# Kernel optimization log

Hardware: AMD Instinct MI355X
Metric: run time of the kernel (lower is better)

Reference implementation:

```python
import jax, jax.numpy as jnp
import numpy as np

B, S, D, H = 16, 4096, 1024, 1024
VOCAB = 512
EMB_DIM = 3


def setup_inputs() -> dict:
    key = jax.random.key(0)
    ks = jax.random.split(key, 12)
    sd = 1.0 / np.sqrt(D)
    sh = 1.0 / np.sqrt(H)
    return {
        "hs": jax.random.normal(ks[0], (B, S, D), dtype=jnp.float32),
        "ht_k": jax.random.normal(ks[1], (B, D), dtype=jnp.float32),
        "hm_k": jax.random.normal(ks[2], (B, H), dtype=jnp.float32),
        "Ws_w": jax.random.uniform(ks[3], (H, D), jnp.float32, -sd, sd),
        "Ws_b": jax.random.uniform(ks[4], (H,), jnp.float32, -sd, sd),
        "Wt_w": jax.random.uniform(ks[5], (H, D), jnp.float32, -sd, sd),
        "Wt_b": jax.random.uniform(ks[6], (H,), jnp.float32, -sd, sd),
        "Wr_w": jax.random.uniform(ks[7], (H, H), jnp.float32, -sh, sh),
        "Wr_b": jax.random.uniform(ks[8], (H,), jnp.float32, -sh, sh),
        "We_w": jax.random.uniform(ks[9], (H,), jnp.float32, -sh, sh),
        "We_b": jax.random.uniform(ks[10], (1,), jnp.float32, -sh, sh),
        "emb_table": jax.random.normal(ks[11], (VOCAB * VOCAB, EMB_DIM), dtype=jnp.float32),
        "entity_lambda": jnp.array([0.3, 0.5, 0.2], dtype=jnp.float32),
        "hs_i": jax.random.randint(jax.random.fold_in(key, 100), (B, S), 0, VOCAB),
        "ht_k_i": jax.random.randint(jax.random.fold_in(key, 101), (B,), 0, VOCAB),
    }


def reference(hs, ht_k, hm_k, Ws_w, Ws_b, Wt_w, Wt_b, Wr_w, Wr_b, We_w, We_b,
              emb_table, entity_lambda, hs_i, ht_k_i):
    # Projections
    W_hs = jnp.einsum('bsd,hd->bsh', hs, Ws_w) + Ws_b          # [B,S,H]
    W_ht = (ht_k @ Wt_w.T + Wt_b)[:, None, :]                   # [B,1,H]
    W_hm = (hm_k @ Wr_w.T + Wr_b)[:, None, :]                   # [B,1,H]
    # Additive attention score
    W_sum = jnp.tanh(W_hs + W_ht + W_hm) @ We_w + We_b[0]       # [B,S]
    # Relative-position bias: gather then contract with lambda
    rel_pos = hs_i * VOCAB + ht_k_i[:, None]                    # [B,S]
    rel_value = emb_table[rel_pos] @ entity_lambda              # [B,S]
    W_sum = W_sum + rel_value
    # Softmax over sequence, weighted sum of projected source states
    W_softmax = jax.nn.softmax(W_sum, axis=1)                   # [B,S]
    alpha = jnp.einsum('bs,bsh->bh', W_softmax, W_hs)           # [B,H]
    return alpha
```

## Files before the change

kernel.cpp:

```cpp
#include <hip/hip_runtime.h>
#include <hip/hip_bf16.h>
#include <cstdint>
#include <cstddef>

typedef __attribute__((ext_vector_type(4))) float f32x4;
typedef __attribute__((ext_vector_type(8))) short short8;

#define S_LEN 4096
#define D_DIM 1024
#define H_DIM 1024
#define B_SZ  16
#define M_TOT (B_SZ * S_LEN)
#define NT 32

__device__ __forceinline__ unsigned short f2bf(float f) {
  unsigned int u = __float_as_uint(f);
  u += 0x7fffu + ((u >> 16) & 1u);
  return (unsigned short)(u >> 16);
}

__device__ __forceinline__ void gload_lds16(void* lds, const void* g) {
  __builtin_amdgcn_global_load_lds(
      (const __attribute__((address_space(1))) unsigned int*)g,
      (__attribute__((address_space(3))) unsigned int*)lds, 16, 0, 0);
}

__device__ __forceinline__ float tanh_fast(float x) {
  return 1.0f - 2.0f / (1.0f + __expf(2.0f * x));
}

#define WAITV(N) asm volatile("s_waitcnt vmcnt(" #N ")" ::: "memory")
#define BAR() __builtin_amdgcn_s_barrier()

__global__ void cvt_hs_kernel(const float* __restrict__ w,
                              unsigned short* __restrict__ o) {
  size_t i = ((size_t)blockIdx.x * 256 + threadIdx.x) * 8;
  float4 v0 = *(const float4*)(w + i);
  float4 v1 = *(const float4*)(w + i + 4);
  union { unsigned short us[8]; short8 v; } pk;
  pk.us[0] = f2bf(v0.x); pk.us[1] = f2bf(v0.y);
  pk.us[2] = f2bf(v0.z); pk.us[3] = f2bf(v0.w);
  pk.us[4] = f2bf(v1.x); pk.us[5] = f2bf(v1.y);
  pk.us[6] = f2bf(v1.z); pk.us[7] = f2bf(v1.w);
  *(short8*)(o + i) = pk.v;
}

__global__ void cvt_w_kernel(const float* __restrict__ w,
                             unsigned short* __restrict__ o) {
  int i = (blockIdx.x * 256 + threadIdx.x) * 8;
  float4 v0 = *(const float4*)(w + i);
  float4 v1 = *(const float4*)(w + i + 4);
  union { unsigned short us[8]; short8 v; } pk;
  pk.us[0] = f2bf(v0.x); pk.us[1] = f2bf(v0.y);
  pk.us[2] = f2bf(v0.z); pk.us[3] = f2bf(v0.w);
  pk.us[4] = f2bf(v1.x); pk.us[5] = f2bf(v1.y);
  pk.us[6] = f2bf(v1.z); pk.us[7] = f2bf(v1.w);
  *(short8*)(o + i) = pk.v;
}

__global__ void prep_c_kernel(const float* __restrict__ ht,
                              const float* __restrict__ hm,
                              const float* __restrict__ Wt_w,
                              const float* __restrict__ Wt_b,
                              const float* __restrict__ Wr_w,
                              const float* __restrict__ Wr_b,
                              float* __restrict__ cvec) {
  int gw = blockIdx.x * 4 + (threadIdx.x >> 6);
  int lane = threadIdx.x & 63;
  int b = gw >> 10;
  int h = gw & 1023;
  const float* a1 = ht + b * D_DIM;
  const float* w1 = Wt_w + (size_t)h * D_DIM;
  const float* a2 = hm + b * H_DIM;
  const float* w2 = Wr_w + (size_t)h * H_DIM;
  float acc = 0.f;
#pragma unroll
  for (int i = 0; i < 4; ++i) {
    int d = lane * 4 + i * 256;
    float4 x1 = *(const float4*)(a1 + d);
    float4 y1 = *(const float4*)(w1 + d);
    float4 x2 = *(const float4*)(a2 + d);
    float4 y2 = *(const float4*)(w2 + d);
    acc += x1.x * y1.x + x1.y * y1.y + x1.z * y1.z + x1.w * y1.w;
    acc += x2.x * y2.x + x2.y * y2.y + x2.z * y2.z + x2.w * y2.w;
  }
#pragma unroll
  for (int off = 32; off >= 1; off >>= 1) acc += __shfl_xor(acc, off);
  if (lane == 0) cvec[b * H_DIM + h] = acc + Wt_b[h] + Wr_b[h];
}

__device__ __forceinline__ void issue_tile(int kt, int tid,
                                           unsigned short* lA,
                                           unsigned short* lB,
                                           const unsigned short* pA0,
                                           const unsigned short* pA1,
                                           const unsigned short* pB0,
                                           const unsigned short* pB1) {
  const int bq = (kt & 3) * 8192;
  const int ko = kt * 32;
  gload_lds16(&lA[bq + tid * 8], pA0 + ko);
  gload_lds16(&lA[bq + 4096 + tid * 8], pA1 + ko);
  gload_lds16(&lB[bq + tid * 8], pB0 + ko);
  gload_lds16(&lB[bq + 4096 + tid * 8], pB1 + ko);
}

__device__ __forceinline__ void read_frags(const unsigned short* bufA,
                                           const unsigned short* bufB,
                                           int aoff0, int boff0,
                                           short8 (&fa)[8], short8 (&fb)[4]) {
#pragma unroll
  for (int ni = 0; ni < 4; ++ni)
    fb[ni] = *(const short8*)(bufB + boff0 + ni * 512);
#pragma unroll
  for (int mi = 0; mi < 8; ++mi)
    fa[mi] = *(const short8*)(bufA + aoff0 + mi * 512);
}

__device__ __forceinline__ void mfma32(const short8 (&fa)[8],
                                       const short8 (&fb)[4],
                                       f32x4 (&acc)[8][4]) {
  __builtin_amdgcn_s_setprio(1);
#pragma unroll
  for (int mi = 0; mi < 8; ++mi)
#pragma unroll
    for (int ni = 0; ni < 4; ++ni)
      acc[mi][ni] = __builtin_amdgcn_mfma_f32_16x16x32_bf16(
          fa[mi], fb[ni], acc[mi][ni], 0, 0, 0);
  __builtin_amdgcn_s_setprio(0);
}

__global__ __launch_bounds__(512, 2) void score_gemm2_kernel(
    const unsigned short* __restrict__ hsb,
    const unsigned short* __restrict__ Wsb,
    const float* __restrict__ cvec,
    const float* __restrict__ We_w,
    float* __restrict__ score_part) {
  extern __shared__ unsigned short dynls[];
  unsigned short* lA = dynls;
  unsigned short* lB = dynls + 32768;
  __shared__ float scorebuf[4][256];

  const int tid = threadIdx.x;
  const int lane = tid & 63;
  const int wave = tid >> 6;
  const int wm = wave >> 2;
  const int wn = wave & 3;
  const int l15 = lane & 15;
  const int lg = lane >> 4;

  int d = blockIdx.x;
  int tileid = (d & 7) * 128 + (d >> 3);
  const int mtile = tileid >> 2;
  const int nc = tileid & 3;
  const int m0 = mtile * 256;
  const int n0 = nc * 256;
  const int b = m0 >> 12;

  const int r0 = tid >> 2;
  const int r1 = 128 + r0;
  const int sp = tid & 3;
  const int c0 = (sp ^ ((r0 >> 1) & 3)) * 8;
  const int c1 = (sp ^ ((r1 >> 1) & 3)) * 8;
  const unsigned short* pA0 = hsb + (size_t)(m0 + r0) * D_DIM + c0;
  const unsigned short* pA1 = hsb + (size_t)(m0 + r1) * D_DIM + c1;
  const unsigned short* pB0 = Wsb + (size_t)(n0 + r0) * D_DIM + c0;
  const unsigned short* pB1 = Wsb + (size_t)(n0 + r1) * D_DIM + c1;

  const int arow0 = wm * 128 + l15;
  const int aoff0 = arow0 * 32 + (lg ^ ((arow0 >> 1) & 3)) * 8;
  const int brow0 = wn * 64 + l15;
  const int boff0 = brow0 * 32 + (lg ^ ((brow0 >> 1) & 3)) * 8;

  f32x4 acc[8][4];
#pragma unroll
  for (int i = 0; i < 8; ++i)
#pragma unroll
    for (int j = 0; j < 4; ++j) acc[i][j] = (f32x4){0.f, 0.f, 0.f, 0.f};

  short8 fa0[8], fb0[4], fa1[8], fb1[4];

  issue_tile(0, tid, lA, lB, pA0, pA1, pB0, pB1);
  issue_tile(1, tid, lA, lB, pA0, pA1, pB0, pB1);
  issue_tile(2, tid, lA, lB, pA0, pA1, pB0, pB1);
  WAITV(4);
  BAR();
  read_frags(lA, lB, aoff0, boff0, fa0, fb0);

  for (int kt = 0; kt < NT - 4; kt += 2) {
    issue_tile(kt + 3, tid, lA, lB, pA0, pA1, pB0, pB1);
    {
      int bq = ((kt + 1) & 3) * 8192;
      read_frags(lA + bq, lB + bq, aoff0, boff0, fa1, fb1);
    }
    mfma32(fa0, fb0, acc);
    WAITV(4);
    BAR();
    issue_tile(kt + 4, tid, lA, lB, pA0, pA1, pB0, pB1);
    {
      int bq = ((kt + 2) & 3) * 8192;
      read_frags(lA + bq, lB + bq, aoff0, boff0, fa0, fb0);
    }
    mfma32(fa1, fb1, acc);
    WAITV(4);
    BAR();
  }
  issue_tile(NT - 1, tid, lA, lB, pA0, pA1, pB0, pB1);
  {
    int bq = ((NT - 3) & 3) * 8192;
    read_frags(lA + bq, lB + bq, aoff0, boff0, fa1, fb1);
  }
  mfma32(fa0, fb0, acc);
  WAITV(4);
  BAR();
  {
    int bq = ((NT - 2) & 3) * 8192;
    read_frags(lA + bq, lB + bq, aoff0, boff0, fa0, fb0);
  }
  mfma32(fa1, fb1, acc);
  WAITV(0);
  BAR();
  {
    int bq = ((NT - 1) & 3) * 8192;
    read_frags(lA + bq, lB + bq, aoff0, boff0, fa1, fb1);
  }
  mfma32(fa0, fb0, acc);
  mfma32(fa1, fb1, acc);

  float chv[4], whv[4];
#pragma unroll
  for (int ni = 0; ni < 4; ++ni) {
    int h = n0 + wn * 64 + ni * 16 + l15;
    chv[ni] = cvec[b * H_DIM + h];
    whv[ni] = We_w[h];
  }
#pragma unroll
  for (int mi = 0; mi < 8; ++mi)
#pragma unroll
    for (int r = 0; r < 4; ++r) {
      float s = 0.f;
#pragma unroll
      for (int ni = 0; ni < 4; ++ni)
        s += tanh_fast(acc[mi][ni][r] + chv[ni]) * whv[ni];
      s += __shfl_xor(s, 1);
      s += __shfl_xor(s, 2);
      s += __shfl_xor(s, 4);
      s += __shfl_xor(s, 8);
      if (l15 == 0) scorebuf[wn][wm * 128 + mi * 16 + lg * 4 + r] = s;
    }
  __syncthreads();
  if (tid < 256) {
    float s = scorebuf[0][tid] + scorebuf[1][tid] + scorebuf[2][tid] +
              scorebuf[3][tid];
    score_part[(size_t)nc * M_TOT + m0 + tid] = s;
  }
}

__global__ __launch_bounds__(256) void score_gemm_fp32_kernel(
    const float* __restrict__ hs,
    const unsigned short* __restrict__ Wsb,
    const float* __restrict__ cvec,
    const float* __restrict__ We_w,
    float* __restrict__ score_part) {
  __shared__ __align__(16) unsigned short lA[128 * 64];
  __shared__ __align__(16) unsigned short lB[128 * 64];
  __shared__ float scorebuf[2][128];

  const int tid = threadIdx.x;
  const int lane = tid & 63;
  const int wave = tid >> 6;
  const int wr = wave >> 1;
  const int wc = wave & 1;
  const int mtile = blockIdx.x;
  const int gy = blockIdx.y;
  const int m0 = mtile * 128;
  const int b = mtile >> 5;
  const int l15 = lane & 15;
  const int lg = lane >> 4;

  float rowsum[4][4];
#pragma unroll
  for (int i = 0; i < 4; ++i)
#pragma unroll
    for (int j = 0; j < 4; ++j) rowsum[i][j] = 0.f;

  for (int ncq = gy * 4; ncq < gy * 4 + 4; ++ncq) {
    const int n0 = ncq * 128;
    f32x4 acc[4][4];
#pragma unroll
    for (int i = 0; i < 4; ++i)
#pragma unroll
      for (int j = 0; j < 4; ++j) acc[i][j] = (f32x4){0.f, 0.f, 0.f, 0.f};

    for (int k0 = 0; k0 < D_DIM; k0 += 64) {
#pragma unroll
      for (int r = 0; r < 4; ++r) {
        int s = tid + r * 256;
        int row = s >> 3, sl = s & 7;
        int src = sl ^ (row & 7);
        gload_lds16(&lB[s * 8], Wsb + (size_t)(n0 + row) * D_DIM + k0 + src * 8);
      }
      float4 a0[4], a1[4];
#pragma unroll
      for (int r = 0; r < 4; ++r) {
        int s = tid + r * 256;
        int row = s >> 3, sl = s & 7;
        int src = sl ^ (row & 7);
        const float* ga = hs + (size_t)(m0 + row) * D_DIM + k0 + src * 8;
        a0[r] = *(const float4*)ga;
        a1[r] = *(const float4*)(ga + 4);
      }
#pragma unroll
      for (int r = 0; r < 4; ++r) {
        int s = tid + r * 256;
        union { unsigned short us[8]; short8 v; } pk;
        pk.us[0] = f2bf(a0[r].x); pk.us[1] = f2bf(a0[r].y);
        pk.us[2] = f2bf(a0[r].z); pk.us[3] = f2bf(a0[r].w);
        pk.us[4] = f2bf(a1[r].x); pk.us[5] = f2bf(a1[r].y);
        pk.us[6] = f2bf(a1[r].z); pk.us[7] = f2bf(a1[r].w);
        *(short8*)(&lA[s * 8]) = pk.v;
      }
      __syncthreads();
#pragma unroll
      for (int kf = 0; kf < 2; ++kf) {
        short8 af[4], bfr[4];
        int cgrp = kf * 4 + lg;
#pragma unroll
        for (int mi = 0; mi < 4; ++mi) {
          int row = wr * 64 + mi * 16 + l15;
          af[mi] = *(const short8*)&lA[row * 64 + (cgrp ^ (row & 7)) * 8];
        }
#pragma unroll
        for (int ni = 0; ni < 4; ++ni) {
          int row = wc * 64 + ni * 16 + l15;
          bfr[ni] = *(const short8*)&lB[row * 64 + (cgrp ^ (row & 7)) * 8];
        }
#pragma unroll
        for (int mi = 0; mi < 4; ++mi)
#pragma unroll
          for (int ni = 0; ni < 4; ++ni)
            acc[mi][ni] = __builtin_amdgcn_mfma_f32_16x16x32_bf16(
                af[mi], bfr[ni], acc[mi][ni], 0, 0, 0);
      }
      __syncthreads();
    }
#pragma unroll
    for (int ni = 0; ni < 4; ++ni) {
      int h = n0 + wc * 64 + ni * 16 + l15;
      float ch = cvec[b * H_DIM + h];
      float wh = We_w[h];
#pragma unroll
      for (int mi = 0; mi < 4; ++mi)
#pragma unroll
        for (int r2 = 0; r2 < 4; ++r2)
          rowsum[mi][r2] += tanh_fast(acc[mi][ni][r2] + ch) * wh;
    }
  }
#pragma unroll
  for (int mi = 0; mi < 4; ++mi)
#pragma unroll
    for (int r2 = 0; r2 < 4; ++r2) {
      float v = rowsum[mi][r2];
      v += __shfl_xor(v, 1);
      v += __shfl_xor(v, 2);
      v += __shfl_xor(v, 4);
      v += __shfl_xor(v, 8);
      rowsum[mi][r2] = v;
    }
  if (l15 == 0) {
#pragma unroll
    for (int mi = 0; mi < 4; ++mi)
#pragma unroll
      for (int r2 = 0; r2 < 4; ++r2)
        scorebuf[wc][wr * 64 + mi * 16 + lg * 4 + r2] = rowsum[mi][r2];
  }
  __syncthreads();
  if (tid < 128) {
    score_part[(size_t)gy * M_TOT + m0 + tid] =
        scorebuf[0][tid] + scorebuf[1][tid];
  }
}

__global__ void softmax_kernel(const float* __restrict__ part,
                               const int* __restrict__ hs_i,
                               const int* __restrict__ ht_i,
                               const float* __restrict__ emb,
                               const float* __restrict__ lam,
                               float* __restrict__ wout, int nparts) {
  int b = blockIdx.x;
  int tid = threadIdx.x;
  float lam0 = lam[0], lam1 = lam[1], lam2 = lam[2];
  int tk = ht_i[b];
  float xs[16];
  float mx = -1e30f;
#pragma unroll
  for (int i = 0; i < 16; ++i) {
    int s = tid + i * 256;
    size_t m = (size_t)b * S_LEN + s;
    float x = 0.f;
    for (int g = 0; g < nparts; ++g) x += part[(size_t)g * M_TOT + m];
    int idx = hs_i[m] * 512 + tk;
    const float* e = emb + (size_t)idx * 3;
    x += e[0] * lam0 + e[1] * lam1 + e[2] * lam2;
    xs[i] = x;
    mx = fmaxf(mx, x);
  }
  __shared__ float redm[4];
  __shared__ float reds[4];
#pragma unroll
  for (int off = 32; off >= 1; off >>= 1) mx = fmaxf(mx, __shfl_xor(mx, off));
  if ((tid & 63) == 0) redm[tid >> 6] = mx;
  __syncthreads();
  mx = fmaxf(fmaxf(redm[0], redm[1]), fmaxf(redm[2], redm[3]));
  float sum = 0.f;
#pragma unroll
  for (int i = 0; i < 16; ++i) {
    xs[i] = __expf(xs[i] - mx);
    sum += xs[i];
  }
#pragma unroll
  for (int off = 32; off >= 1; off >>= 1) sum += __shfl_xor(sum, off);
  if ((tid & 63) == 0) reds[tid >> 6] = sum;
  __syncthreads();
  sum = reds[0] + reds[1] + reds[2] + reds[3];
  float inv = 1.0f / sum;
#pragma unroll
  for (int i = 0; i < 16; ++i)
    wout[(size_t)b * S_LEN + tid + i * 256] = xs[i] * inv;
}

__global__ void wsum_bf16_kernel(const unsigned short* __restrict__ hsb,
                                 const float* __restrict__ w,
                                 float* __restrict__ u) {
  int bx = blockIdx.x;
  int b = bx >> 5;
  int sc = bx & 31;
  int tid = threadIdx.x;
  int dcol = tid * 4;
  int s0 = sc * 128;
  const unsigned short* base = hsb + ((size_t)b * S_LEN + s0) * D_DIM + dcol;
  const float* wrow = w + (size_t)b * S_LEN + s0;
  float4 acc = {0.f, 0.f, 0.f, 0.f};
#pragma unroll 4
  for (int i = 0; i < 128; ++i) {
    float ww = wrow[i];
    ushort2 v01 = *(const ushort2*)(base + (size_t)i * D_DIM);
    ushort2 v23 = *(const ushort2*)(base + (size_t)i * D_DIM + 2);
    acc.x += ww * __uint_as_float((unsigned int)v01.x << 16);
    acc.y += ww * __uint_as_float((unsigned int)v01.y << 16);
    acc.z += ww * __uint_as_float((unsigned int)v23.x << 16);
    acc.w += ww * __uint_as_float((unsigned int)v23.y << 16);
  }
  atomicAdd(&u[b * D_DIM + dcol + 0], acc.x);
  atomicAdd(&u[b * D_DIM + dcol + 1], acc.y);
  atomicAdd(&u[b * D_DIM + dcol + 2], acc.z);
  atomicAdd(&u[b * D_DIM + dcol + 3], acc.w);
}

__global__ void wsum_kernel(const float* __restrict__ hs,
                            const float* __restrict__ w,
                            float* __restrict__ u) {
  int bx = blockIdx.x;
  int b = bx >> 5;
  int sc = bx & 31;
  int tid = threadIdx.x;
  int dcol = tid * 4;
  int s0 = sc * 128;
  const float* base = hs + ((size_t)b * S_LEN + s0) * D_DIM + dcol;
  const float* wrow = w + (size_t)b * S_LEN + s0;
  float4 acc = {0.f, 0.f, 0.f, 0.f};
#pragma unroll 4
  for (int i = 0; i < 128; ++i) {
    float ww = wrow[i];
    float4 v = *(const float4*)(base + (size_t)i * D_DIM);
    acc.x += ww * v.x;
    acc.y += ww * v.y;
    acc.z += ww * v.z;
    acc.w += ww * v.w;
  }
  atomicAdd(&u[b * D_DIM + dcol + 0], acc.x);
  atomicAdd(&u[b * D_DIM + dcol + 1], acc.y);
  atomicAdd(&u[b * D_DIM + dcol + 2], acc.z);
  atomicAdd(&u[b * D_DIM + dcol + 3], acc.w);
}

__global__ void alpha_kernel(const float* __restrict__ u,
                             const float* __restrict__ Ws_w,
                             const float* __restrict__ Ws_b,
                             float* __restrict__ out) {
  int gw = blockIdx.x * 4 + (threadIdx.x >> 6);
  int lane = threadIdx.x & 63;
  int b = gw >> 10;
  int h = gw & 1023;
  const float* ur = u + b * D_DIM;
  const float* wrow = Ws_w + (size_t)h * D_DIM;
  float acc = 0.f;
#pragma unroll
  for (int i = 0; i < 4; ++i) {
    int dcol = lane * 4 + i * 256;
    float4 x = *(const float4*)(ur + dcol);
    float4 y = *(const float4*)(wrow + dcol);
    acc += x.x * y.x + x.y * y.y + x.z * y.z + x.w * y.w;
  }
#pragma unroll
  for (int off = 32; off >= 1; off >>= 1) acc += __shfl_xor(acc, off);
  if (lane == 0) out[b * H_DIM + h] = acc + Ws_b[h];
}

extern "C" void kernel_launch(void* const* d_in, const int* in_sizes, int n_in,
                              void* d_out, int out_size, void* d_ws,
                              size_t ws_size, hipStream_t stream) {
  const float* hs = (const float*)d_in[0];
  const float* ht_k = (const float*)d_in[1];
  const float* hm_k = (const float*)d_in[2];
  const float* Ws_w = (const float*)d_in[3];
  const float* Ws_b = (const float*)d_in[4];
  const float* Wt_w = (const float*)d_in[5];
  const float* Wt_b = (const float*)d_in[6];
  const float* Wr_w = (const float*)d_in[7];
  const float* Wr_b = (const float*)d_in[8];
  const float* We_w = (const float*)d_in[9];
  const float* emb = (const float*)d_in[11];
  const float* lam = (const float*)d_in[12];
  const int* hs_i = (const int*)d_in[13];
  const int* ht_i = (const int*)d_in[14];
  float* out = (float*)d_out;

  const size_t HSB = (size_t)M_TOT * D_DIM * 2;
  const size_t FAST_NEEDED = HSB + 2097152 + 1048576 + 262144 + 65536 + 65536;

  char* ws = (char*)d_ws;
  if (ws_size >= FAST_NEEDED) {
    unsigned short* hsb = (unsigned short*)ws;
    unsigned short* Wsb = (unsigned short*)(ws + HSB);
    float* part = (float*)(ws + HSB + 2097152);
    float* wgt = (float*)(ws + HSB + 2097152 + 1048576);
    float* u = (float*)(ws + HSB + 2097152 + 1048576 + 262144);
    float* cvec = (float*)(ws + HSB + 2097152 + 1048576 + 262144 + 65536);

    hipFuncSetAttribute((const void*)score_gemm2_kernel,
                        hipFuncAttributeMaxDynamicSharedMemorySize, 131072);

    cvt_hs_kernel<<<32768, 256, 0, stream>>>(hs, hsb);
    cvt_w_kernel<<<512, 256, 0, stream>>>(Ws_w, Wsb);
    prep_c_kernel<<<4096, 256, 0, stream>>>(ht_k, hm_k, Wt_w, Wt_b, Wr_w,
                                            Wr_b, cvec);
    score_gemm2_kernel<<<1024, 512, 131072, stream>>>(hsb, Wsb, cvec, We_w,
                                                      part);
    softmax_kernel<<<16, 256, 0, stream>>>(part, hs_i, ht_i, emb, lam, wgt, 4);
    hipMemsetAsync(u, 0, B_SZ * D_DIM * sizeof(float), stream);
    wsum_bf16_kernel<<<512, 256, 0, stream>>>(hsb, wgt, u);
    alpha_kernel<<<4096, 256, 0, stream>>>(u, Ws_w, Ws_b, out);
    return;
  }

  unsigned short* Wsb = (unsigned short*)(ws);
  float* cvec = (float*)(ws + 2097152);
  float* part = (float*)(ws + 2097152 + 65536);
  float* wgt = (float*)(ws + 2097152 + 65536 + 524288);
  float* u = (float*)(ws + 2097152 + 65536 + 524288 + 262144);

  cvt_w_kernel<<<512, 256, 0, stream>>>(Ws_w, Wsb);
  prep_c_kernel<<<4096, 256, 0, stream>>>(ht_k, hm_k, Wt_w, Wt_b, Wr_w, Wr_b,
                                          cvec);
  dim3 g2(512, 2);
  score_gemm_fp32_kernel<<<g2, 256, 0, stream>>>(hs, Wsb, cvec, We_w, part);
  softmax_kernel<<<16, 256, 0, stream>>>(part, hs_i, ht_i, emb, lam, wgt, 2);
  hipMemsetAsync(u, 0, B_SZ * D_DIM * sizeof(float), stream);
  wsum_kernel<<<512, 256, 0, stream>>>(hs, wgt, u);
  alpha_kernel<<<4096, 256, 0, stream>>>(u, Ws_w, Ws_b, out);
}
```

Before: 299.3 us.

## Restructure score GEMM main loop to double-buffered K=64 stages with interleaved loads

Replaces the 4-deep ring of K=32 tiles with a 2-buffer scheme of K=64 stages (16 iterations), using a new XOR swizzle over 8 column chunks. Each stage is split into four quarter-steps, each issuing a slice of the next stage's global-to-LDS loads, reading fragments, waiting on lgkmcnt and running 16 MFMAs. The goal is to spread load issue evenly across the compute and cut register pressure from double fragment sets. In exchange it adds many more barriers per stage and a full vmcnt(0) drain at the end of each stage, which shortens the prefetch distance.

```diff
diff --git a/kernel.cpp b/kernel.cpp
--- a/kernel.cpp
+++ b/kernel.cpp
@@ -11,7 +11,6 @@
 #define H_DIM 1024
 #define B_SZ  16
 #define M_TOT (B_SZ * S_LEN)
-#define NT 32
 
 __device__ __forceinline__ unsigned short f2bf(float f) {
   unsigned int u = __float_as_uint(f);
@@ -29,8 +28,12 @@
   return 1.0f - 2.0f / (1.0f + __expf(2.0f * x));
 }
 
-#define WAITV(N) asm volatile("s_waitcnt vmcnt(" #N ")" ::: "memory")
 #define BAR() __builtin_amdgcn_s_barrier()
+#define LGKM0()                                            \
+  do {                                                     \
+    asm volatile("s_waitcnt lgkmcnt(0)" ::: "memory");     \
+    __builtin_amdgcn_sched_barrier(0);                     \
+  } while (0)
 
 __global__ void cvt_hs_kernel(const float* __restrict__ w,
                               unsigned short* __restrict__ o) {
@@ -89,47 +92,44 @@
   if (lane == 0) cvec[b * H_DIM + h] = acc + Wt_b[h] + Wr_b[h];
 }
 
-__device__ __forceinline__ void issue_tile(int kt, int tid,
-                                           unsigned short* lA,
-                                           unsigned short* lB,
-                                           const unsigned short* pA0,
-                                           const unsigned short* pA1,
-                                           const unsigned short* pB0,
-                                           const unsigned short* pB1) {
-  const int bq = (kt & 3) * 8192;
-  const int ko = kt * 32;
-  gload_lds16(&lA[bq + tid * 8], pA0 + ko);
-  gload_lds16(&lA[bq + 4096 + tid * 8], pA1 + ko);
-  gload_lds16(&lB[bq + tid * 8], pB0 + ko);
-  gload_lds16(&lB[bq + 4096 + tid * 8], pB1 + ko);
-}
-
-__device__ __forceinline__ void read_frags(const unsigned short* bufA,
-                                           const unsigned short* bufB,
-                                           int aoff0, int boff0,
-                                           short8 (&fa)[8], short8 (&fb)[4]) {
-#pragma unroll
-  for (int ni = 0; ni < 4; ++ni)
-    fb[ni] = *(const short8*)(bufB + boff0 + ni * 512);
-#pragma unroll
-  for (int mi = 0; mi < 8; ++mi)
-    fa[mi] = *(const short8*)(bufA + aoff0 + mi * 512);
-}
-
-__device__ __forceinline__ void mfma32(const short8 (&fa)[8],
-                                       const short8 (&fb)[4],
-                                       f32x4 (&acc)[8][4]) {
-  __builtin_amdgcn_s_setprio(1);
-#pragma unroll
-  for (int mi = 0; mi < 8; ++mi)
-#pragma unroll
-    for (int ni = 0; ni < 4; ++ni)
-      acc[mi][ni] = __builtin_amdgcn_mfma_f32_16x16x32_bf16(
-          fa[mi], fb[ni], acc[mi][ni], 0, 0, 0);
-  __builtin_amdgcn_s_setprio(0);
-}
-
-__global__ __launch_bounds__(512, 2) void score_gemm2_kernel(
+#define STG_A(nb, h, ss)                                                  \
+  do {                                                                    \
+    gload_lds16(lA + (nb)*16384 + (h)*8192 + dst0,                        \
+                gA + (h)*131072 + (ss)*64);                               \
+    gload_lds16(lA + (nb)*16384 + (h)*8192 + dst1,                        \
+                gA + (h)*131072 + 65536 + (ss)*64);                       \
+  } while (0)
+#define STG_B(nb, h, ss)                                                  \
+  do {                                                                    \
+    gload_lds16(lB + (nb)*16384 + (h)*8192 + dst0,                        \
+                gB + (h)*131072 + (ss)*64);                               \
+    gload_lds16(lB + (nb)*16384 + (h)*8192 + dst1,                        \
+                gB + (h)*131072 + 65536 + (ss)*64);                       \
+  } while (0)
+
+#define RDA_LO(OFF)                                                       \
+  { _Pragma("unroll") for (int mi = 0; mi < 4; ++mi)                      \
+      fa[mi] = *(const short8*)(bA + (OFF) + mi * 1024); }
+#define RDA_HI(OFF)                                                       \
+  { _Pragma("unroll") for (int mi = 0; mi < 4; ++mi)                      \
+      fa[mi] = *(const short8*)(bA + (OFF) + 4096 + mi * 1024); }
+#define RDB(FB, OFF)                                                      \
+  { _Pragma("unroll") for (int ni = 0; ni < 4; ++ni)                      \
+      FB[ni] = *(const short8*)(bB + (OFF) + ni * 1024); }
+
+#define MM16(MIB, FB)                                                     \
+  {                                                                       \
+    __builtin_amdgcn_s_setprio(1);                                        \
+    _Pragma("unroll") for (int mi = 0; mi < 4; ++mi) {                    \
+      _Pragma("unroll") for (int ni = 0; ni < 4; ++ni) {                  \
+        acc[(MIB) + mi][ni] = __builtin_amdgcn_mfma_f32_16x16x32_bf16(    \
+            fa[mi], FB[ni], acc[(MIB) + mi][ni], 0, 0, 0);                \
+      }                                                                   \
+    }                                                                     \
+    __builtin_amdgcn_s_setprio(0);                                        \
+  }
+
+__global__ __launch_bounds__(512, 2) void score_gemm3_kernel(
     const unsigned short* __restrict__ hsb,
     const unsigned short* __restrict__ Wsb,
     const float* __restrict__ cvec,
@@ -156,20 +156,18 @@
   const int n0 = nc * 256;
   const int b = m0 >> 12;
 
-  const int r0 = tid >> 2;
-  const int r1 = 128 + r0;
-  const int sp = tid & 3;
-  const int c0 = (sp ^ ((r0 >> 1) & 3)) * 8;
-  const int c1 = (sp ^ ((r1 >> 1) & 3)) * 8;
-  const unsigned short* pA0 = hsb + (size_t)(m0 + r0) * D_DIM + c0;
-  const unsigned short* pA1 = hsb + (size_t)(m0 + r1) * D_DIM + c1;
-  const unsigned short* pB0 = Wsb + (size_t)(n0 + r0) * D_DIM + c0;
-  const unsigned short* pB1 = Wsb + (size_t)(n0 + r1) * D_DIM + c1;
-
-  const int arow0 = wm * 128 + l15;
-  const int aoff0 = arow0 * 32 + (lg ^ ((arow0 >> 1) & 3)) * 8;
-  const int brow0 = wn * 64 + l15;
-  const int boff0 = brow0 * 32 + (lg ^ ((brow0 >> 1) & 3)) * 8;
+  const int tr = tid >> 3;
+  const int tc = tid & 7;
+  const int scol = ((tc ^ (tr & 7)) << 3);
+  const unsigned short* gA = hsb + (size_t)(m0 + tr) * 1024 + scol;
+  const unsigned short* gB = Wsb + (size_t)(n0 + tr) * 1024 + scol;
+  const int dst0 = tid * 8;
+  const int dst1 = 4096 + tid * 8;
+
+  const int aoff0 = (wm * 128 + l15) * 64 + ((lg ^ (l15 & 7)) << 3);
+  const int aoff1 = (wm * 128 + l15) * 64 + (((4 + lg) ^ (l15 & 7)) << 3);
+  const int boff0 = (wn * 64 + l15) * 64 + ((lg ^ (l15 & 7)) << 3);
+  const int boff1 = (wn * 64 + l15) * 64 + (((4 + lg) ^ (l15 & 7)) << 3);
 
   f32x4 acc[8][4];
 #pragma unroll
@@ -177,54 +175,48 @@
 #pragma unroll
     for (int j = 0; j < 4; ++j) acc[i][j] = (f32x4){0.f, 0.f, 0.f, 0.f};
 
-  short8 fa0[8], fb0[4], fa1[8], fb1[4];
-
-  issue_tile(0, tid, lA, lB, pA0, pA1, pB0, pB1);
-  issue_tile(1, tid, lA, lB, pA0, pA1, pB0, pB1);
-  issue_tile(2, tid, lA, lB, pA0, pA1, pB0, pB1);
-  WAITV(4);
+  STG_A(0, 0, 0);
+  STG_A(0, 1, 0);
+  STG_B(0, 0, 0);
+  STG_B(0, 1, 0);
+  asm volatile("s_waitcnt vmcnt(0)" ::: "memory");
   BAR();
-  read_frags(lA, lB, aoff0, boff0, fa0, fb0);
-
-  for (int kt = 0; kt < NT - 4; kt += 2) {
-    issue_tile(kt + 3, tid, lA, lB, pA0, pA1, pB0, pB1);
-    {
-      int bq = ((kt + 1) & 3) * 8192;
-      read_frags(lA + bq, lB + bq, aoff0, boff0, fa1, fb1);
-    }
-    mfma32(fa0, fb0, acc);
-    WAITV(4);
-    BAR();
-    issue_tile(kt + 4, tid, lA, lB, pA0, pA1, pB0, pB1);
-    {
-      int bq = ((kt + 2) & 3) * 8192;
-      read_frags(lA + bq, lB + bq, aoff0, boff0, fa0, fb0);
-    }
-    mfma32(fa1, fb1, acc);
-    WAITV(4);
-    BAR();
-  }
-  issue_tile(NT - 1, tid, lA, lB, pA0, pA1, pB0, pB1);
-  {
-    int bq = ((NT - 3) & 3) * 8192;
-    read_frags(lA + bq, lB + bq, aoff0, boff0, fa1, fb1);
-  }
-  mfma32(fa0, fb0, acc);
-  WAITV(4);
-  BAR();
-  {
-    int bq = ((NT - 2) & 3) * 8192;
-    read_frags(lA + bq, lB + bq, aoff0, boff0, fa0, fb0);
-  }
-  mfma32(fa1, fb1, acc);
-  WAITV(0);
-  BAR();
-  {
-    int bq = ((NT - 1) & 3) * 8192;
-    read_frags(lA + bq, lB + bq, aoff0, boff0, fa1, fb1);
-  }
-  mfma32(fa0, fb0, acc);
-  mfma32(fa1, fb1, acc);
+
+#pragma unroll 2
+  for (int s = 0; s < 16; ++s) {
+    const unsigned short* bA = lA + (s & 1) * 16384;
+    const unsigned short* bB = lB + (s & 1) * 16384;
+    const int nb = (s & 1) ^ 1;
+    const bool st = (s < 15);
+    short8 fa[4], fb0[4], fb1[4];
+    RDA_LO(aoff0);
+    RDB(fb0, boff0);
+    if (st) STG_A(nb, 0, s + 1);
+    BAR();
+    LGKM0();
+    MM16(0, fb0);
+    BAR();
+    RDA_HI(aoff0);
+    if (st) STG_A(nb, 1, s + 1);
+    BAR();
+    LGKM0();
+    MM16(4, fb0);
+    BAR();
+    RDA_LO(aoff1);
+    RDB(fb1, boff1);
+    if (st) STG_B(nb, 0, s + 1);
+    BAR();
+    LGKM0();
+    MM16(0, fb1);
+    BAR();
+    RDA_HI(aoff1);
+    if (st) STG_B(nb, 1, s + 1);
+    BAR();
+    LGKM0();
+    MM16(4, fb1);
+    asm volatile("s_waitcnt vmcnt(0)" ::: "memory");
+    BAR();
+  }
 
   float chv[4], whv[4];
 #pragma unroll
@@ -537,14 +529,14 @@
     float* u = (float*)(ws + HSB + 2097152 + 1048576 + 262144);
     float* cvec = (float*)(ws + HSB + 2097152 + 1048576 + 262144 + 65536);
 
-    hipFuncSetAttribute((const void*)score_gemm2_kernel,
+    hipFuncSetAttribute((const void*)score_gemm3_kernel,
                         hipFuncAttributeMaxDynamicSharedMemorySize, 131072);
 
     cvt_hs_kernel<<<32768, 256, 0, stream>>>(hs, hsb);
     cvt_w_kernel<<<512, 256, 0, stream>>>(Ws_w, Wsb);
     prep_c_kernel<<<4096, 256, 0, stream>>>(ht_k, hm_k, Wt_w, Wt_b, Wr_w,
                                             Wr_b, cvec);
-    score_gemm2_kernel<<<1024, 512, 131072, stream>>>(hsb, Wsb, cvec, We_w,
+    score_gemm3_kernel<<<1024, 512, 131072, stream>>>(hsb, Wsb, cvec, We_w,
                                                       part);
     softmax_kernel<<<16, 256, 0, stream>>>(part, hs_i, ht_i, emb, lam, wgt, 4);
     hipMemsetAsync(u, 0, B_SZ * D_DIM * sizeof(float), stream);
```

Result: faster. 288.5 us (-3.6%).
